# Performance work log

Hardware: AMD Instinct MI355X
Metric: run time of the kernel (lower is better)

Reference implementation:

```python
import jax, jax.numpy as jnp
import numpy as np

DIM = 128      # dim
NC = 50000     # number of code nodes
NE = 100000    # number of hyperedges (visits)
T = 800000     # total flattened (code, edge) incidences
GAMMA = 0.5


def setup_inputs() -> dict:
    key = jax.random.key(0)
    ks = jax.random.split(key, 18)
    d = DIM
    s = 1.0 / np.sqrt(d)
    return {
        "H_e": jax.random.normal(ks[0], (NE, d), jnp.float32),
        "H_c": jax.random.normal(ks[1], (NC, d), jnp.float32),
        "timestamps": jax.random.uniform(ks[2], (NE,), jnp.float32),
        "W_e": jax.random.normal(ks[3], (d, d), jnp.float32) * s,
        "be_lin": jax.random.normal(ks[4], (d,), jnp.float32) * s,
        "b_e": jnp.zeros((d,), jnp.float32),
        "W_c": jax.random.normal(ks[5], (d, d), jnp.float32) * s,
        "bc_lin": jax.random.normal(ks[6], (d,), jnp.float32) * s,
        "b_c": jnp.zeros((d,), jnp.float32),
        "W_t": jax.random.normal(ks[7], (d, d), jnp.float32) * s,
        "b_t": jax.random.normal(ks[8], (d,), jnp.float32) * s,
        "W_g": jax.random.normal(ks[9], (d, d), jnp.float32) * s,
        "b_g": jax.random.normal(ks[10], (d,), jnp.float32) * s,
        "omega": jax.random.normal(ks[11], (d // 2,), jnp.float32),
        "W_t2v": jax.random.normal(ks[12], (d, d), jnp.float32) * s,
        "b_t2v": jax.random.normal(ks[13], (d,), jnp.float32) * s,
        "edge_ids": jax.random.randint(ks[14], (T,), 0, NE, jnp.int32),
        "seg_ids": jnp.sort(jax.random.randint(ks[15], (T,), 0, NC, jnp.int32)),
    }


def reference(H_e, H_c, timestamps, W_e, be_lin, b_e, W_c, bc_lin, b_c,
              W_t, b_t, W_g, b_g, omega, W_t2v, b_t2v, edge_ids, seg_ids):
    n_codes = H_c.shape[0]
    # --- gather variable-length neighbor sets (flattened segments) ---
    hes = H_e[edge_ids]                      # [T, d]
    hcs = H_c[seg_ids]                       # [T, d]
    tes = timestamps[edge_ids]               # [T]
    # --- Time2Vec ---
    tw = tes[:, None] * omega                # [T, d//2]
    t2v = jnp.concatenate([jnp.cos(tw), jnp.sin(tw)], axis=-1) @ W_t2v + b_t2v  # [T, d]
    # --- score: <proj_e * proj_c, sigmoid(linear_t(alpha_e))> ---
    proj_e = hes @ W_e + be_lin + b_e        # [T, d]
    proj_c = hcs @ W_c + bc_lin + b_c        # [T, d]
    gate = jax.nn.sigmoid(t2v @ W_t + b_t)   # [T, d]
    scores = jnp.sum(proj_e * proj_c * gate, axis=-1)  # [T]
    # --- segment softmax over each code's neighbor set ---
    smax = jax.ops.segment_max(scores, seg_ids, num_segments=n_codes)
    smax = jnp.where(jnp.isfinite(smax), smax, 0.0)
    ex = jnp.exp(scores - smax[seg_ids])
    denom = jax.ops.segment_sum(ex, seg_ids, num_segments=n_codes)
    attn = ex / jnp.maximum(denom, 1e-30)[seg_ids]      # [T]
    # --- weighted aggregate of g(h_e), scatter back to codes ---
    msg = attn[:, None] * (hes @ W_g + b_g)             # [T, d]
    agg = jax.ops.segment_sum(msg, seg_ids, num_segments=n_codes)  # [Nc, d]
    cnt = jax.ops.segment_sum(jnp.ones_like(scores), seg_ids, num_segments=n_codes)
    has_edge = (cnt > 0)[:, None]
    return jnp.where(has_edge, GAMMA * agg + (1.0 - GAMMA) * H_c, H_c)
```

## Files before the change

kernel.cpp:

```cpp
#include <hip/hip_runtime.h>
#include <math.h>

#define DIM   128
#define NC_   50000
#define NE_   100000
#define T_    800000

typedef __attribute__((ext_vector_type(8))) _Float16 f16x8;
typedef __attribute__((ext_vector_type(2))) _Float16 f16x2;
typedef __attribute__((ext_vector_type(4))) float f32x4;

__device__ __forceinline__ float sigmoidf_(float x) {
    return 1.f / (1.f + __expf(-x));
}

__device__ __forceinline__ float dot2f(f16x2 a, f16x2 b, float c) {
#if defined(__has_builtin) && __has_builtin(__builtin_amdgcn_fdot2)
    return __builtin_amdgcn_fdot2(a, b, c, false);
#else
    return c + (float)a[0] * (float)b[0] + (float)a[1] * (float)b[1];
#endif
}

__global__ __launch_bounds__(128)
void k_combine(const float* __restrict__ W_t2v, const float* __restrict__ W_t,
               const float* __restrict__ b_t2v, const float* __restrict__ b_t,
               float* __restrict__ W_tt, float* __restrict__ b_tt) {
    const int i = blockIdx.x, j = threadIdx.x;
    float acc = 0.f;
    if (i < DIM) {
        for (int k = 0; k < DIM; ++k) acc = fmaf(W_t2v[i*DIM+k], W_t[k*DIM+j], acc);
        W_tt[i*DIM+j] = acc;
    } else {
        for (int k = 0; k < DIM; ++k) acc = fmaf(b_t2v[k], W_t[k*DIM+j], acc);
        b_tt[j] = acc + b_t[j];
    }
}

__global__ __launch_bounds__(64)
void k_pack(const float* __restrict__ s0, const float* __restrict__ s1,
            const float* __restrict__ s2, const float* __restrict__ s3,
            _Float16* __restrict__ d0, _Float16* __restrict__ d1,
            _Float16* __restrict__ d2, _Float16* __restrict__ d3) {
    const float* srcs[4] = {s0, s1, s2, s3};
    _Float16* dsts[4] = {d0, d1, d2, d3};
    const float* src = srcs[blockIdx.y];
    _Float16* dst = dsts[blockIdx.y];
    const int b = blockIdx.x;
    const int nt = b >> 2, kb = b & 3;
    const int lane = threadIdx.x;
    const int n  = nt * 16 + (lane & 15);
    const int k0 = kb * 32 + 8 * (lane >> 4);
    const size_t off = ((size_t)(nt * 4 + kb) * 64 + lane) * 8;
    #pragma unroll
    for (int e = 0; e < 8; ++e)
        dst[off + e] = (_Float16)src[(size_t)(k0 + e) * DIM + n];
}

__global__ __launch_bounds__(256)
void k_starts(const int* __restrict__ seg, int* __restrict__ start) {
    int t = blockIdx.x * 256 + threadIdx.x;
    if (t > T_) return;
    if (t < T_) {
        int s  = seg[t];
        int sp = (t > 0) ? seg[t-1] : -1;
        for (int c = sp + 1; c <= s; ++c) start[c] = t;
    } else {
        int sp = seg[T_-1];
        for (int c = sp + 1; c <= NC_; ++c) start[c] = T_;
    }
}

__device__ __forceinline__ void split8h(const float* xs, f16x8* hi, f16x8* lo) {
    #pragma unroll
    for (int e = 0; e < 8; ++e) {
        _Float16 h = (_Float16)xs[e];
        (*hi)[e] = h;
        (*lo)[e] = (_Float16)(xs[e] - (float)h);
    }
}

__device__ __forceinline__ void stage_lds(_Float16* lds, const _Float16* __restrict__ g) {
    const int tid = threadIdx.x;
    #pragma unroll
    for (int i = 0; i < 8; ++i)
        ((uint4*)lds)[tid + i * 256] = ((const uint4*)g)[tid + i * 256];
}

__device__ __forceinline__ void mfma2(f16x8 ahi, f16x8 alo, const _Float16* lds_bp,
                                      f32x4* acc) {
    f16x8 b = *(const f16x8*)lds_bp;
    *acc = __builtin_amdgcn_mfma_f32_16x16x32_f16(ahi, b, *acc, 0, 0, 0);
    *acc = __builtin_amdgcn_mfma_f32_16x16x32_f16(alo, b, *acc, 0, 0, 0);
}

__global__ __launch_bounds__(256)
void k_edge(const float* __restrict__ H_e, const float* __restrict__ ts,
            const _Float16* __restrict__ packWe, const _Float16* __restrict__ packWtt,
            const float* __restrict__ be_lin, const float* __restrict__ b_e,
            const float* __restrict__ b_tt, const float* __restrict__ omega,
            _Float16* __restrict__ u16, _Float16* __restrict__ He16) {
    __shared__ __align__(16) _Float16 ldsW[16384];
    const int tid  = threadIdx.x;
    const int lane = tid & 63;
    const int q    = lane & 15, g = lane >> 4;
    const int brow = blockIdx.x * 64 + (tid >> 6) * 16;
    const int arow = brow + q;
    const bool valid = arow < NE_;
    const float* ap = H_e + (size_t)(valid ? arow : 0) * DIM;
    const float te  = valid ? ts[arow] : 0.f;

    stage_lds(ldsW, packWe);

    f32x4 accU[8], accG[8];
    #pragma unroll
    for (int i = 0; i < 8; ++i) {
        accU[i] = (f32x4){0.f, 0.f, 0.f, 0.f};
        accG[i] = (f32x4){0.f, 0.f, 0.f, 0.f};
    }
    __syncthreads();

    #pragma unroll
    for (int kb = 0; kb < 4; ++kb) {
        const int k0 = kb * 32 + 8 * g;
        float xs[8];
        if (valid) {
            float4 x0 = *(const float4*)(ap + k0);
            float4 x1 = *(const float4*)(ap + k0 + 4);
            xs[0]=x0.x; xs[1]=x0.y; xs[2]=x0.z; xs[3]=x0.w;
            xs[4]=x1.x; xs[5]=x1.y; xs[6]=x1.z; xs[7]=x1.w;
        } else {
            #pragma unroll
            for (int e = 0; e < 8; ++e) xs[e] = 0.f;
        }
        f16x8 ahi, alo;
        split8h(xs, &ahi, &alo);
        if (valid) *(f16x8*)&He16[(size_t)arow * DIM + k0] = ahi;
        #pragma unroll
        for (int nt = 0; nt < 8; ++nt)
            mfma2(ahi, alo, &ldsW[((nt * 4 + kb) * 64 + lane) * 8], &accU[nt]);
    }

    __syncthreads();
    stage_lds(ldsW, packWtt);
    __syncthreads();

    #pragma unroll
    for (int kb = 0; kb < 4; ++kb) {
        const int k0 = kb * 32 + 8 * g;
        float ys[8];
        #pragma unroll
        for (int e = 0; e < 8; ++e) {
            const int k = k0 + e;
            float x = te * omega[k & 63];
            float s, c;
            __sincosf(x, &s, &c);
            ys[e] = (k < 64) ? c : s;
        }
        f16x8 thi, tlo;
        split8h(ys, &thi, &tlo);
        #pragma unroll
        for (int nt = 0; nt < 8; ++nt)
            mfma2(thi, tlo, &ldsW[((nt * 4 + kb) * 64 + lane) * 8], &accG[nt]);
    }

    #pragma unroll
    for (int nt = 0; nt < 8; ++nt) {
        const int col = nt * 16 + q;
        const float bu = be_lin[col] + b_e[col];
        const float bg = b_tt[col];
        #pragma unroll
        for (int reg = 0; reg < 4; ++reg) {
            const int e = brow + 4 * g + reg;
            if (e < NE_) {
                float val = (accU[nt][reg] + bu) * sigmoidf_(accG[nt][reg] + bg);
                u16[(size_t)e * DIM + col] = (_Float16)val;
            }
        }
    }
}

__global__ __launch_bounds__(256)
void k_code(const float* __restrict__ H_c, const _Float16* __restrict__ packWc,
            const float* __restrict__ bc_lin, const float* __restrict__ b_c,
            float* __restrict__ pc) {
    __shared__ __align__(16) _Float16 ldsW[16384];
    const int tid  = threadIdx.x;
    const int lane = tid & 63;
    const int q    = lane & 15, g = lane >> 4;
    const int brow = blockIdx.x * 64 + (tid >> 6) * 16;
    const int arow = brow + q;
    const bool valid = arow < NC_;
    const float* ap = H_c + (size_t)(valid ? arow : 0) * DIM;

    stage_lds(ldsW, packWc);

    f32x4 acc[8];
    #pragma unroll
    for (int i = 0; i < 8; ++i) acc[i] = (f32x4){0.f, 0.f, 0.f, 0.f};
    __syncthreads();

    #pragma unroll
    for (int kb = 0; kb < 4; ++kb) {
        const int k0 = kb * 32 + 8 * g;
        float xs[8];
        if (valid) {
            float4 x0 = *(const float4*)(ap + k0);
            float4 x1 = *(const float4*)(ap + k0 + 4);
            xs[0]=x0.x; xs[1]=x0.y; xs[2]=x0.z; xs[3]=x0.w;
            xs[4]=x1.x; xs[5]=x1.y; xs[6]=x1.z; xs[7]=x1.w;
        } else {
            #pragma unroll
            for (int e = 0; e < 8; ++e) xs[e] = 0.f;
        }
        f16x8 ahi, alo;
        split8h(xs, &ahi, &alo);
        #pragma unroll
        for (int nt = 0; nt < 8; ++nt)
            mfma2(ahi, alo, &ldsW[((nt * 4 + kb) * 64 + lane) * 8], &acc[nt]);
    }

    #pragma unroll
    for (int nt = 0; nt < 8; ++nt) {
        const int col = nt * 16 + q;
        const float bc = bc_lin[col] + b_c[col];
        #pragma unroll
        for (int reg = 0; reg < 4; ++reg) {
            const int c = brow + 4 * g + reg;
            if (c < NC_) pc[(size_t)c * DIM + col] = acc[nt][reg] + bc;
        }
    }
}

__global__ __launch_bounds__(256)
void k_seg(const _Float16* __restrict__ u16, float* __restrict__ pcv,
           const _Float16* __restrict__ He16, const int* __restrict__ edge_ids,
           const int* __restrict__ start) {
    const int lane = threadIdx.x & 63;
    const int c = blockIdx.x * 4 + (threadIdx.x >> 6);
    if (c >= NC_) return;
    const int lo = start[c], hi = start[c + 1];
    const int g = lane >> 3;
    const int q = lane & 7;
    const int j0 = q * 16;

    f16x2 pch[8];
    #pragma unroll
    for (int i = 0; i < 8; ++i) {
        float2 pp = *(const float2*)&pcv[(size_t)c * DIM + j0 + 2 * i];
        f16x2 h; h[0] = (_Float16)pp.x; h[1] = (_Float16)pp.y;
        pch[i] = h;
    }

    float M = -INFINITY, S = 0.f;
    float acc[16];
    #pragma unroll
    for (int i = 0; i < 16; ++i) acc[i] = 0.f;

    for (int base = lo; base < hi; base += 64) {
        const int n = min(64, hi - base);
        const int eid = (base + lane < hi) ? edge_ids[base + lane] : 0;
        const int niter = (n + 7) >> 3;
        float msc = -INFINITY;

        for (int jj = 0; jj < niter; ++jj) {
            const int s = 8 * jj + g;
            const int e = __shfl(eid, s);
            float p = 0.f;
            if (s < n) {
                union { uint4 r[2]; f16x2 h2[8]; } uu;
                const _Float16* up = &u16[(size_t)e * DIM + j0];
                uu.r[0] = *(const uint4*)up;
                uu.r[1] = *(const uint4*)(up + 8);
                #pragma unroll
                for (int i = 0; i < 8; ++i) p = dot2f(uu.h2[i], pch[i], p);
            }
            p += __shfl_xor(p, 1);
            p += __shfl_xor(p, 2);
            p += __shfl_xor(p, 4);
            if (q == jj && s < n) msc = p;
        }

        float cm = msc;
        #pragma unroll
        for (int off = 32; off; off >>= 1) cm = fmaxf(cm, __shfl_xor(cm, off));
        const float nM = fmaxf(M, cm);
        const float scale = __expf(M - nM);
        const float pi = __expf(msc - nM);
        float ss = pi;
        #pragma unroll
        for (int off = 32; off; off >>= 1) ss += __shfl_xor(ss, off);
        S = S * scale + ss;
        #pragma unroll
        for (int i = 0; i < 16; ++i) acc[i] *= scale;
        M = nM;

        for (int jj = 0; jj < niter; ++jj) {
            const int s = 8 * jj + g;
            const int e = __shfl(eid, s);
            const float p = __shfl(pi, 8 * g + jj);
            if (s < n) {
                union { uint4 r[2]; f16x8 h8[2]; } hh;
                const _Float16* hp = &He16[(size_t)e * DIM + j0];
                hh.r[0] = *(const uint4*)hp;
                hh.r[1] = *(const uint4*)(hp + 8);
                #pragma unroll
                for (int i = 0; i < 8; ++i) {
                    acc[i]     = fmaf(p, (float)hh.h8[0][i], acc[i]);
                    acc[8 + i] = fmaf(p, (float)hh.h8[1][i], acc[8 + i]);
                }
            }
        }
    }

    #pragma unroll
    for (int off = 8; off <= 32; off <<= 1) {
        #pragma unroll
        for (int i = 0; i < 16; ++i) acc[i] += __shfl_xor(acc[i], off);
    }

    if (g == 0) {
        const float inv = (hi > lo) ? 1.f / fmaxf(S, 1e-30f) : 0.f;
        #pragma unroll
        for (int v = 0; v < 4; ++v) {
            float4 o;
            o.x = acc[4*v+0] * inv; o.y = acc[4*v+1] * inv;
            o.z = acc[4*v+2] * inv; o.w = acc[4*v+3] * inv;
            *(float4*)&pcv[(size_t)c * DIM + j0 + 4 * v] = o;
        }
    }
}

__global__ __launch_bounds__(256)
void k_out(const float* __restrict__ v, const _Float16* __restrict__ packWg,
           const float* __restrict__ b_g, const float* __restrict__ H_c,
           const int* __restrict__ start, float* __restrict__ out) {
    __shared__ __align__(16) _Float16 ldsW[16384];
    const int tid  = threadIdx.x;
    const int lane = tid & 63;
    const int q    = lane & 15, g = lane >> 4;
    const int brow = blockIdx.x * 64 + (tid >> 6) * 16;
    const int arow = brow + q;
    const bool valid = arow < NC_;
    const float* ap = v + (size_t)(valid ? arow : 0) * DIM;

    stage_lds(ldsW, packWg);

    f32x4 acc[8];
    #pragma unroll
    for (int i = 0; i < 8; ++i) acc[i] = (f32x4){0.f, 0.f, 0.f, 0.f};
    __syncthreads();

    #pragma unroll
    for (int kb = 0; kb < 4; ++kb) {
        const int k0 = kb * 32 + 8 * g;
        float xs[8];
        if (valid) {
            float4 x0 = *(const float4*)(ap + k0);
            float4 x1 = *(const float4*)(ap + k0 + 4);
            xs[0]=x0.x; xs[1]=x0.y; xs[2]=x0.z; xs[3]=x0.w;
            xs[4]=x1.x; xs[5]=x1.y; xs[6]=x1.z; xs[7]=x1.w;
        } else {
            #pragma unroll
            for (int e = 0; e < 8; ++e) xs[e] = 0.f;
        }
        f16x8 ahi, alo;
        split8h(xs, &ahi, &alo);
        #pragma unroll
        for (int nt = 0; nt < 8; ++nt)
            mfma2(ahi, alo, &ldsW[((nt * 4 + kb) * 64 + lane) * 8], &acc[nt]);
    }

    #pragma unroll
    for (int reg = 0; reg < 4; ++reg) {
        const int c = brow + 4 * g + reg;
        if (c >= NC_) continue;
        const bool has = start[c + 1] > start[c];
        #pragma unroll
        for (int nt = 0; nt < 8; ++nt) {
            const int col = nt * 16 + q;
            const float hc = H_c[(size_t)c * DIM + col];
            float o = has ? 0.5f * (acc[nt][reg] + b_g[col]) + 0.5f * hc : hc;
            out[(size_t)c * DIM + col] = o;
        }
    }
}

extern "C" void kernel_launch(void* const* d_in, const int* in_sizes, int n_in,
                              void* d_out, int out_size, void* d_ws, size_t ws_size,
                              hipStream_t stream) {
    const float* H_e    = (const float*)d_in[0];
    const float* H_c    = (const float*)d_in[1];
    const float* ts     = (const float*)d_in[2];
    const float* W_e    = (const float*)d_in[3];
    const float* be_lin = (const float*)d_in[4];
    const float* b_e    = (const float*)d_in[5];
    const float* W_c    = (const float*)d_in[6];
    const float* bc_lin = (const float*)d_in[7];
    const float* b_c    = (const float*)d_in[8];
    const float* W_t    = (const float*)d_in[9];
    const float* b_t    = (const float*)d_in[10];
    const float* W_g    = (const float*)d_in[11];
    const float* b_g    = (const float*)d_in[12];
    const float* omega  = (const float*)d_in[13];
    const float* W_t2v  = (const float*)d_in[14];
    const float* b_t2v  = (const float*)d_in[15];
    const int* edge_ids = (const int*)d_in[16];
    const int* seg_ids  = (const int*)d_in[17];
    float* out = (float*)d_out;

    char* w = (char*)d_ws;
    _Float16* u16  = (_Float16*)w; w += (size_t)NE_ * DIM * sizeof(_Float16);
    _Float16* He16 = (_Float16*)w; w += (size_t)NE_ * DIM * sizeof(_Float16);
    float* pcv  = (float*)w;  w += (size_t)NC_ * DIM * sizeof(float);
    int* start  = (int*)w;    w += (((size_t)(NC_ + 1) * sizeof(int)) + 255) & ~(size_t)255;
    float* W_tt = (float*)w;  w += (size_t)DIM * DIM * sizeof(float);
    float* b_tt = (float*)w;  w += 1024;
    _Float16* packWe  = (_Float16*)w; w += 16384 * sizeof(_Float16);
    _Float16* packWtt = (_Float16*)w; w += 16384 * sizeof(_Float16);
    _Float16* packWc  = (_Float16*)w; w += 16384 * sizeof(_Float16);
    _Float16* packWg  = (_Float16*)w; w += 16384 * sizeof(_Float16);
    if ((size_t)(w - (char*)d_ws) > ws_size) return;

    k_combine<<<dim3(DIM + 1), dim3(128), 0, stream>>>(W_t2v, W_t, b_t2v, b_t, W_tt, b_tt);
    k_pack<<<dim3(32, 4), dim3(64), 0, stream>>>(W_e, W_tt, W_c, W_g,
                                                 packWe, packWtt, packWc, packWg);
    k_starts<<<dim3((T_ + 1 + 255) / 256), dim3(256), 0, stream>>>(seg_ids, start);
    k_edge<<<dim3((NE_ + 63) / 64), dim3(256), 0, stream>>>(H_e, ts, packWe, packWtt,
                                                            be_lin, b_e, b_tt, omega,
                                                            u16, He16);
    k_code<<<dim3((NC_ + 63) / 64), dim3(256), 0, stream>>>(H_c, packWc, bc_lin, b_c, pcv);
    k_seg<<<dim3((NC_ + 3) / 4), dim3(256), 0, stream>>>(u16, pcv, He16, edge_ids, start);
    k_out<<<dim3((NC_ + 63) / 64), dim3(256), 0, stream>>>(pcv, packWg, b_g, H_c, start, out);
}
```

Before: 148.6 us.

## Interleave gated edge projection and fp16 H_e into one record per edge

The two per-edge fp16 arrays (gated projection u and H_e copy) are merged into a single 256-element record per edge. In the segment kernel, the first 32 neighbors of each chunk load both halves in the score pass and keep the H_e half in registers, so the aggregation pass does not re-gather them. The goal is fewer scattered gathers and better locality, since both halves of a record sit next to each other. The cost is extra register pressure from holding eight uint4 per lane, which may lower occupancy.

After: 151.1 us. Within noise of the previous version (+1.6%).

```diff
diff --git a/kernel.cpp b/kernel.cpp
--- a/kernel.cpp
+++ b/kernel.cpp
@@ -99,7 +99,7 @@
             const _Float16* __restrict__ packWe, const _Float16* __restrict__ packWtt,
             const float* __restrict__ be_lin, const float* __restrict__ b_e,
             const float* __restrict__ b_tt, const float* __restrict__ omega,
-            _Float16* __restrict__ u16, _Float16* __restrict__ He16) {
+            _Float16* __restrict__ rec) {
     __shared__ __align__(16) _Float16 ldsW[16384];
     const int tid  = threadIdx.x;
     const int lane = tid & 63;
@@ -135,7 +135,7 @@
         }
         f16x8 ahi, alo;
         split8h(xs, &ahi, &alo);
-        if (valid) *(f16x8*)&He16[(size_t)arow * DIM + k0] = ahi;
+        if (valid) *(f16x8*)&rec[(size_t)arow * 256 + 128 + k0] = ahi;
         #pragma unroll
         for (int nt = 0; nt < 8; ++nt)
             mfma2(ahi, alo, &ldsW[((nt * 4 + kb) * 64 + lane) * 8], &accU[nt]);
@@ -174,7 +174,7 @@
             const int e = brow + 4 * g + reg;
             if (e < NE_) {
                 float val = (accU[nt][reg] + bu) * sigmoidf_(accG[nt][reg] + bg);
-                u16[(size_t)e * DIM + col] = (_Float16)val;
+                rec[(size_t)e * 256 + col] = (_Float16)val;
             }
         }
     }
@@ -233,9 +233,8 @@
 }
 
 __global__ __launch_bounds__(256)
-void k_seg(const _Float16* __restrict__ u16, float* __restrict__ pcv,
-           const _Float16* __restrict__ He16, const int* __restrict__ edge_ids,
-           const int* __restrict__ start) {
+void k_seg(const _Float16* __restrict__ rec, float* __restrict__ pcv,
+           const int* __restrict__ edge_ids, const int* __restrict__ start) {
     const int lane = threadIdx.x & 63;
     const int c = blockIdx.x * 4 + (threadIdx.x >> 6);
     if (c >= NC_) return;
@@ -262,16 +261,21 @@
         const int eid = (base + lane < hi) ? edge_ids[base + lane] : 0;
         const int niter = (n + 7) >> 3;
         float msc = -INFINITY;
-
-        for (int jj = 0; jj < niter; ++jj) {
+        uint4 heA[4], heB[4];
+
+        #pragma unroll
+        for (int jj = 0; jj < 4; ++jj) {
             const int s = 8 * jj + g;
             const int e = __shfl(eid, s);
             float p = 0.f;
+            heA[jj] = make_uint4(0,0,0,0); heB[jj] = make_uint4(0,0,0,0);
             if (s < n) {
+                const _Float16* rp = &rec[(size_t)e * 256 + j0];
                 union { uint4 r[2]; f16x2 h2[8]; } uu;
-                const _Float16* up = &u16[(size_t)e * DIM + j0];
-                uu.r[0] = *(const uint4*)up;
-                uu.r[1] = *(const uint4*)(up + 8);
+                uu.r[0] = *(const uint4*)rp;
+                uu.r[1] = *(const uint4*)(rp + 8);
+                heA[jj] = *(const uint4*)(rp + 128);
+                heB[jj] = *(const uint4*)(rp + 136);
                 #pragma unroll
                 for (int i = 0; i < 8; ++i) p = dot2f(uu.h2[i], pch[i], p);
             }
@@ -280,6 +284,23 @@
             p += __shfl_xor(p, 4);
             if (q == jj && s < n) msc = p;
         }
+        for (int jj = 4; jj < niter; ++jj) {
+            const int s = 8 * jj + g;
+            const int e = __shfl(eid, s);
+            float p = 0.f;
+            if (s < n) {
+                const _Float16* rp = &rec[(size_t)e * 256 + j0];
+                union { uint4 r[2]; f16x2 h2[8]; } uu;
+                uu.r[0] = *(const uint4*)rp;
+                uu.r[1] = *(const uint4*)(rp + 8);
+                #pragma unroll
+                for (int i = 0; i < 8; ++i) p = dot2f(uu.h2[i], pch[i], p);
+            }
+            p += __shfl_xor(p, 1);
+            p += __shfl_xor(p, 2);
+            p += __shfl_xor(p, 4);
+            if (q == jj && s < n) msc = p;
+        }
 
         float cm = msc;
         #pragma unroll
@@ -295,13 +316,27 @@
         for (int i = 0; i < 16; ++i) acc[i] *= scale;
         M = nM;
 
-        for (int jj = 0; jj < niter; ++jj) {
+        #pragma unroll
+        for (int jj = 0; jj < 4; ++jj) {
+            const int s = 8 * jj + g;
+            const float p = __shfl(pi, 8 * g + jj);
+            if (s < n) {
+                union { uint4 r[2]; f16x8 h8[2]; } hh;
+                hh.r[0] = heA[jj]; hh.r[1] = heB[jj];
+                #pragma unroll
+                for (int i = 0; i < 8; ++i) {
+                    acc[i]     = fmaf(p, (float)hh.h8[0][i], acc[i]);
+                    acc[8 + i] = fmaf(p, (float)hh.h8[1][i], acc[8 + i]);
+                }
+            }
+        }
+        for (int jj = 4; jj < niter; ++jj) {
             const int s = 8 * jj + g;
             const int e = __shfl(eid, s);
             const float p = __shfl(pi, 8 * g + jj);
             if (s < n) {
+                const _Float16* hp = &rec[(size_t)e * 256 + 128 + j0];
                 union { uint4 r[2]; f16x8 h8[2]; } hh;
-                const _Float16* hp = &He16[(size_t)e * DIM + j0];
                 hh.r[0] = *(const uint4*)hp;
                 hh.r[1] = *(const uint4*)(hp + 8);
                 #pragma unroll
@@ -410,8 +445,7 @@
     float* out = (float*)d_out;
 
     char* w = (char*)d_ws;
-    _Float16* u16  = (_Float16*)w; w += (size_t)NE_ * DIM * sizeof(_Float16);
-    _Float16* He16 = (_Float16*)w; w += (size_t)NE_ * DIM * sizeof(_Float16);
+    _Float16* rec  = (_Float16*)w; w += (size_t)NE_ * 256 * sizeof(_Float16);
     float* pcv  = (float*)w;  w += (size_t)NC_ * DIM * sizeof(float);
     int* start  = (int*)w;    w += (((size_t)(NC_ + 1) * sizeof(int)) + 255) & ~(size_t)255;
     float* W_tt = (float*)w;  w += (size_t)DIM * DIM * sizeof(float);
@@ -427,9 +461,8 @@
                                                  packWe, packWtt, packWc, packWg);
     k_starts<<<dim3((T_ + 1 + 255) / 256), dim3(256), 0, stream>>>(seg_ids, start);
     k_edge<<<dim3((NE_ + 63) / 64), dim3(256), 0, stream>>>(H_e, ts, packWe, packWtt,
-                                                            be_lin, b_e, b_tt, omega,
-                                                            u16, He16);
+                                                            be_lin, b_e, b_tt, omega, rec);
     k_code<<<dim3((NC_ + 63) / 64), dim3(256), 0, stream>>>(H_c, packWc, bc_lin, b_c, pcv);
-    k_seg<<<dim3((NC_ + 3) / 4), dim3(256), 0, stream>>>(u16, pcv, He16, edge_ids, start);
+    k_seg<<<dim3((NC_ + 3) / 4), dim3(256), 0, stream>>>(rec, pcv, edge_ids, start);
     k_out<<<dim3((NC_ + 63) / 64), dim3(256), 0, stream>>>(pcv, packWg, b_g, H_c, start, out);
 }
```
